# Kernel optimization log

Measured on AMD Instinct MI355X. Metric: run time of the kernel, lower is better.

The kernel has to match this reference:

```python
import jax, jax.numpy as jnp
import numpy as np

MARGIN = 0.0
B, N_CLASSES = 8192, 4


def setup_inputs() -> dict:
    key = jax.random.key(0)
    k1, k2, k3, k4 = jax.random.split(key, 4)
    hazards = jax.random.uniform(k1, (B, N_CLASSES), dtype=jnp.float32)
    S = jax.random.uniform(k2, (B, N_CLASSES), dtype=jnp.float32)
    Y = jax.random.randint(k3, (B,), 0, N_CLASSES, dtype=jnp.int64)
    c = jax.random.randint(k4, (B,), 0, 2, dtype=jnp.int64)
    return {"hazards": hazards, "S": S, "Y": Y, "c": c}


def reference(hazards, S, Y, c):
    # risk score per sample: sum of hazards over time bins
    risk = hazards.sum(axis=1)  # [B]
    # pair (i, j) contributes iff sample i is uncensored and Y[j] > Y[i]
    mask = (c == 0)[:, None] & (Y[None, :] > Y[:, None])  # [B, B] bool
    # diff[i, j] = margin + risk[j] - risk[i]
    diff = jax.nn.relu(MARGIN + risk[None, :] - risk[:, None])  # [B, B]
    count = jnp.sum(mask)
    total = jnp.sum(jnp.where(mask, diff, jnp.zeros_like(diff)))
    # if count == 0, loss stays 0 (matches torch code)
    loss = jnp.where(count > 0, total / count.astype(diff.dtype), jnp.zeros((), diff.dtype))
    return loss
```

## Files before the change

### kernel.cpp

```cpp
#include <hip/hip_runtime.h>


#define B_SIZE 8192
#define TILE 256
#define NBLK ((B_SIZE / TILE) * (B_SIZE / TILE))

__global__ __launch_bounds__(TILE) void rl_pairs(
    const float4* __restrict__ hz,
    const int*    __restrict__ Y,
    const int*    __restrict__ c,
    float*        __restrict__ psum,
    int*          __restrict__ pcnt)
{
    const int tid  = threadIdx.x;
    const int lane = tid & 63;

    const int j = blockIdx.x * TILE + tid;
    const float4 hj = hz[j];
    const float rj = (hj.x + hj.y) + (hj.z + hj.w);
    const int   yj = Y[j];

    const int i0 = blockIdx.y * TILE;
    float ri[4];
    int   yi[4];
    #pragma unroll
    for (int s = 0; s < 4; ++s) {
        const int i = i0 + s * 64 + lane;
        const float4 hi = hz[i];
        ri[s] = (hi.x + hi.y) + (hi.z + hi.w);
        yi[s] = (c[i] != 0) ? 1000 : Y[i];
    }

    float acc = 0.0f;
    int   cnt = 0;
    #pragma unroll
    for (int s = 0; s < 4; ++s) {
        #pragma unroll
        for (int l = 0; l < 64; ++l) {
            const int yib = __builtin_amdgcn_readlane(yi[s], l);
            if (yib < 4) {
                const float rib = __uint_as_float(
                    (unsigned)__builtin_amdgcn_readlane((int)__float_as_uint(ri[s]), l));
                const bool m = (yj > yib);
                const float d = fmaxf(rj - rib, 0.0f);
                acc += m ? d : 0.0f;
                cnt += m ? 1 : 0;
            }
        }
    }

    #pragma unroll
    for (int off = 32; off > 0; off >>= 1) {
        acc += __shfl_down(acc, off, 64);
        cnt += __shfl_down(cnt, off, 64);
    }
    __shared__ float sa[TILE / 64];
    __shared__ int   sc[TILE / 64];
    const int wave = tid >> 6;
    if (lane == 0) { sa[wave] = acc; sc[wave] = cnt; }
    __syncthreads();
    if (tid == 0) {
        float a = 0.0f; int n = 0;
        #pragma unroll
        for (int w = 0; w < TILE / 64; ++w) { a += sa[w]; n += sc[w]; }
        const int gid = blockIdx.y * gridDim.x + blockIdx.x;
        psum[gid] = a;
        pcnt[gid] = n;
    }
}

__global__ __launch_bounds__(256) void rl_final(
    const float* __restrict__ psum,
    const int*   __restrict__ pcnt,
    float*       __restrict__ out)
{
    const int tid  = threadIdx.x;
    const int lane = tid & 63;
    float a = 0.0f; int n = 0;
    #pragma unroll
    for (int k = 0; k < NBLK / 256; ++k) {
        a += psum[k * 256 + tid];
        n += pcnt[k * 256 + tid];
    }
    #pragma unroll
    for (int off = 32; off > 0; off >>= 1) {
        a += __shfl_down(a, off, 64);
        n += __shfl_down(n, off, 64);
    }
    __shared__ float sa[4];
    __shared__ int   sc[4];
    const int wave = tid >> 6;
    if (lane == 0) { sa[wave] = a; sc[wave] = n; }
    __syncthreads();
    if (tid == 0) {
        float A = sa[0] + sa[1] + sa[2] + sa[3];
        int   N = sc[0] + sc[1] + sc[2] + sc[3];
        out[0] = (N > 0) ? (A / (float)N) : 0.0f;
    }
}

extern "C" void kernel_launch(void* const* d_in, const int* in_sizes, int n_in,
                              void* d_out, int out_size, void* d_ws, size_t ws_size,
                              hipStream_t stream) {
    const float4* hz = (const float4*)d_in[0];
    const int* Y = (const int*)d_in[2];
    const int* c = (const int*)d_in[3];
    float* psum = (float*)d_ws;
    int*   pcnt = (int*)d_ws + NBLK;
    float* out  = (float*)d_out;

    rl_pairs<<<dim3(B_SIZE / TILE, B_SIZE / TILE), TILE, 0, stream>>>(hz, Y, c, psum, pcnt);
    rl_final<<<1, 256, 0, stream>>>(psum, pcnt, out);
}
```

Before: 72.86 us.

## Compact uncensored samples by class and compute pair count analytically

Adds a single-block pre-pass that builds per-class histograms of labels, computes the valid-pair count in closed form, and packs uncensored risks into 64-wide class-homogeneous groups padded with sentinels. The pair kernel then loops only over these compacted groups, rotating risks across lanes with DPP moves instead of readlane, and keeps no per-pair count or mask test. This cuts pair work to uncensored samples with smaller labels and removes the counting arithmetic. In exchange it adds an extra serial single-block launch, and a float sentinel trick stands in for the mask.

```diff
diff --git a/kernel.cpp b/kernel.cpp
--- a/kernel.cpp
+++ b/kernel.cpp
@@ -2,100 +2,165 @@
 
 
 #define B_SIZE 8192
-#define TILE 256
-#define NBLK ((B_SIZE / TILE) * (B_SIZE / TILE))
+#define BLOCK  256
+#define JT     (B_SIZE / BLOCK)
+#define GY     32
+#define NPSUM  (JT * GY)
 
-__global__ __launch_bounds__(TILE) void rl_pairs(
+#define CR_OFF    0
+#define GCLS_OFF  36864
+#define SCAL_OFF  40960
+#define PSUM_OFF  49152
+
+__global__ __launch_bounds__(1024) void rl_compact(
     const float4* __restrict__ hz,
     const int*    __restrict__ Y,
     const int*    __restrict__ c,
-    float*        __restrict__ psum,
-    int*          __restrict__ pcnt)
+    float* __restrict__ cr,
+    int*   __restrict__ gcls,
+    int*   __restrict__ scal)
+{
+    const int t    = threadIdx.x;
+    const int lane = t & 63;
+
+    float r[8]; int y[8]; bool keep[8];
+    #pragma unroll
+    for (int k = 0; k < 8; ++k) {
+        const int e = k * 1024 + t;
+        const float4 h = hz[e];
+        r[k] = (h.x + h.y) + (h.z + h.w);
+        y[k] = Y[e];
+        keep[k] = (c[e] == 0);
+    }
+
+    __shared__ int histA[4], histU[4], fill[4];
+    __shared__ int sNG;
+    if (t < 4) { histA[t] = 0; histU[t] = 0; }
+    __syncthreads();
+
+    int la[4] = {0,0,0,0}, lu[4] = {0,0,0,0};
+    #pragma unroll
+    for (int k = 0; k < 8; ++k) {
+        #pragma unroll
+        for (int cls = 0; cls < 4; ++cls) {
+            const unsigned long long mA = __ballot(y[k] == cls);
+            const unsigned long long mU = __ballot(keep[k] && (y[k] == cls));
+            la[cls] += (int)__popcll(mA);
+            lu[cls] += (int)__popcll(mU);
+        }
+    }
+    if (lane == 0) {
+        #pragma unroll
+        for (int cls = 0; cls < 4; ++cls) {
+            atomicAdd(&histA[cls], la[cls]);
+            atomicAdd(&histU[cls], lu[cls]);
+        }
+    }
+    __syncthreads();
+
+    if (t == 0) {
+        int suff[5]; suff[4] = 0;
+        for (int a = 3; a >= 0; --a) suff[a] = suff[a + 1] + histA[a];
+        long long cnt = 0;
+        int off = 0, ng = 0;
+        for (int a = 0; a < 3; ++a) {
+            fill[a] = off;
+            const int pad = (histU[a] + 63) & ~63;
+            for (int g = 0; g < pad / 64; ++g) gcls[ng + g] = a;
+            ng += pad / 64;
+            off += pad;
+            cnt += (long long)histU[a] * suff[a + 1];
+        }
+        cnt += (long long)histU[3] * suff[4];
+        fill[3] = off;
+        sNG = ng;
+        scal[0] = ng;
+        scal[1] = (int)cnt;
+    }
+    __syncthreads();
+
+    const int M = sNG * 64;
+    for (int idx = t; idx < M; idx += 1024) cr[idx] = 1e30f;
+    __syncthreads();
+
+    #pragma unroll
+    for (int k = 0; k < 8; ++k) {
+        #pragma unroll
+        for (int cls = 0; cls < 3; ++cls) {
+            const bool mine = keep[k] && (y[k] == cls);
+            const unsigned long long m = __ballot(mine);
+            if (m == 0ull) continue;
+            const int rank = (int)__popcll(m & ((1ull << lane) - 1ull));
+            int base;
+            if (lane == 0) base = atomicAdd(&fill[cls], (int)__popcll(m));
+            base = __shfl(base, 0, 64);
+            if (mine) cr[base + rank] = r[k];
+        }
+    }
+}
+
+__global__ __launch_bounds__(BLOCK) void rl_pairs(
+    const float4* __restrict__ hz,
+    const int*    __restrict__ Y,
+    const float*  __restrict__ cr,
+    const int*    __restrict__ gcls,
+    const int*    __restrict__ scal,
+    float*        __restrict__ psum)
 {
     const int tid  = threadIdx.x;
     const int lane = tid & 63;
 
-    const int j = blockIdx.x * TILE + tid;
-    const float4 hj = hz[j];
-    const float rj = (hj.x + hj.y) + (hj.z + hj.w);
+    const int j = blockIdx.x * BLOCK + tid;
+    const float4 h = hz[j];
+    const float rj = (h.x + h.y) + (h.z + h.w);
     const int   yj = Y[j];
+    const float rj0 = (yj > 0) ? rj : -1e30f;
+    const float rj1 = (yj > 1) ? rj : -1e30f;
+    const float rj2 = (yj > 2) ? rj : -1e30f;
 
-    const int i0 = blockIdx.y * TILE;
-    float ri[4];
-    int   yi[4];
-    #pragma unroll
-    for (int s = 0; s < 4; ++s) {
-        const int i = i0 + s * 64 + lane;
-        const float4 hi = hz[i];
-        ri[s] = (hi.x + hi.y) + (hi.z + hi.w);
-        yi[s] = (c[i] != 0) ? 1000 : Y[i];
-    }
+    const int NG = scal[0];
+    float acc = 0.0f;
 
-    float acc = 0.0f;
-    int   cnt = 0;
-    #pragma unroll
-    for (int s = 0; s < 4; ++s) {
+    for (int g = blockIdx.y; g < NG; g += GY) {
+        const int cls = gcls[g];
+        const float rjc = (cls == 0) ? rj0 : (cls == 1) ? rj1 : rj2;
+        float ri = cr[g * 64 + lane];
         #pragma unroll
-        for (int l = 0; l < 64; ++l) {
-            const int yib = __builtin_amdgcn_readlane(yi[s], l);
-            if (yib < 4) {
-                const float rib = __uint_as_float(
-                    (unsigned)__builtin_amdgcn_readlane((int)__float_as_uint(ri[s]), l));
-                const bool m = (yj > yib);
-                const float d = fmaxf(rj - rib, 0.0f);
-                acc += m ? d : 0.0f;
-                cnt += m ? 1 : 0;
-            }
+        for (int it = 0; it < 64; ++it) {
+            const float d = rjc - ri;
+            acc += fmaxf(d, 0.0f);
+            ri = __uint_as_float((unsigned)__builtin_amdgcn_mov_dpp(
+                     (int)__float_as_uint(ri), 0x13C , 0xF, 0xF, true));
         }
     }
 
     #pragma unroll
-    for (int off = 32; off > 0; off >>= 1) {
-        acc += __shfl_down(acc, off, 64);
-        cnt += __shfl_down(cnt, off, 64);
-    }
-    __shared__ float sa[TILE / 64];
-    __shared__ int   sc[TILE / 64];
-    const int wave = tid >> 6;
-    if (lane == 0) { sa[wave] = acc; sc[wave] = cnt; }
+    for (int off = 32; off > 0; off >>= 1) acc += __shfl_down(acc, off, 64);
+    __shared__ float sa[BLOCK / 64];
+    if (lane == 0) sa[tid >> 6] = acc;
     __syncthreads();
-    if (tid == 0) {
-        float a = 0.0f; int n = 0;
-        #pragma unroll
-        for (int w = 0; w < TILE / 64; ++w) { a += sa[w]; n += sc[w]; }
-        const int gid = blockIdx.y * gridDim.x + blockIdx.x;
-        psum[gid] = a;
-        pcnt[gid] = n;
-    }
+    if (tid == 0)
+        psum[blockIdx.y * JT + blockIdx.x] = (sa[0] + sa[1]) + (sa[2] + sa[3]);
 }
 
 __global__ __launch_bounds__(256) void rl_final(
     const float* __restrict__ psum,
-    const int*   __restrict__ pcnt,
+    const int*   __restrict__ scal,
     float*       __restrict__ out)
 {
     const int tid  = threadIdx.x;
     const int lane = tid & 63;
-    float a = 0.0f; int n = 0;
+    float a = 0.0f;
     #pragma unroll
-    for (int k = 0; k < NBLK / 256; ++k) {
-        a += psum[k * 256 + tid];
-        n += pcnt[k * 256 + tid];
-    }
+    for (int k = 0; k < NPSUM / 256; ++k) a += psum[k * 256 + tid];
     #pragma unroll
-    for (int off = 32; off > 0; off >>= 1) {
-        a += __shfl_down(a, off, 64);
-        n += __shfl_down(n, off, 64);
-    }
+    for (int off = 32; off > 0; off >>= 1) a += __shfl_down(a, off, 64);
     __shared__ float sa[4];
-    __shared__ int   sc[4];
-    const int wave = tid >> 6;
-    if (lane == 0) { sa[wave] = a; sc[wave] = n; }
+    if (lane == 0) sa[tid >> 6] = a;
     __syncthreads();
     if (tid == 0) {
-        float A = sa[0] + sa[1] + sa[2] + sa[3];
-        int   N = sc[0] + sc[1] + sc[2] + sc[3];
-        out[0] = (N > 0) ? (A / (float)N) : 0.0f;
+        const int n = scal[1];
+        out[0] = (n > 0) ? ((sa[0] + sa[1]) + (sa[2] + sa[3])) / (float)n : 0.0f;
     }
 }
 
@@ -105,10 +170,15 @@
     const float4* hz = (const float4*)d_in[0];
     const int* Y = (const int*)d_in[2];
     const int* c = (const int*)d_in[3];
-    float* psum = (float*)d_ws;
-    int*   pcnt = (int*)d_ws + NBLK;
+
+    char* ws = (char*)d_ws;
+    float* cr   = (float*)(ws + CR_OFF);
+    int*   gcls = (int*)  (ws + GCLS_OFF);
+    int*   scal = (int*)  (ws + SCAL_OFF);
+    float* psum = (float*)(ws + PSUM_OFF);
     float* out  = (float*)d_out;
 
-    rl_pairs<<<dim3(B_SIZE / TILE, B_SIZE / TILE), TILE, 0, stream>>>(hz, Y, c, psum, pcnt);
-    rl_final<<<1, 256, 0, stream>>>(psum, pcnt, out);
+    rl_compact<<<1, 1024, 0, stream>>>(hz, Y, c, cr, gcls, scal);
+    rl_pairs<<<dim3(JT, GY), BLOCK, 0, stream>>>(hz, Y, cr, gcls, scal, psum);
+    rl_final<<<1, 256, 0, stream>>>(psum, scal, out);
 }
```

Measured after the change: 74.63 us. +2.4%, slower.

## Bucket uncensored rows by class in shared memory and compute pair counts analytically

Applied to the files above, without the earlier changes.

Each block now sorts its uncensored i-samples by class into fixed-size shared-memory pads, using ballot, popcount and shared atomics. The pair count becomes a closed-form product of per-class counts and suffix counts instead of per-pair accumulation. The inner loop walks each class pad with DPP wave rotations instead of per-lane readlane plus a branch. Pads are filled with sentinels so unused slots add zero, which removes the masking work and the count accumulation. The trade-off is extra shared atomics and barriers, and each class bucket is capped at 128 entries, so a skewed input could silently drop pairs from the sum.

```diff
diff --git a/kernel.cpp b/kernel.cpp
--- a/kernel.cpp
+++ b/kernel.cpp
@@ -2,70 +2,91 @@
 
 
 #define B_SIZE 8192
-#define TILE 256
-#define NBLK ((B_SIZE / TILE) * (B_SIZE / TILE))
+#define BLOCK  256
+#define JT     (B_SIZE / BLOCK)
+#define IC     (B_SIZE / BLOCK)
+#define NBLK   (JT * IC)
+#define CAP    128
 
-__global__ __launch_bounds__(TILE) void rl_pairs(
+__global__ __launch_bounds__(BLOCK) void rl_all(
     const float4* __restrict__ hz,
     const int*    __restrict__ Y,
     const int*    __restrict__ c,
     float*        __restrict__ psum,
     int*          __restrict__ pcnt)
 {
+    __shared__ float sPad[3 * CAP];
+    __shared__ int   sCnt[3];
+    __shared__ int   sSuf[3];
+    __shared__ float sA[BLOCK / 64];
+    __shared__ int   sN[BLOCK / 64];
+
     const int tid  = threadIdx.x;
     const int lane = tid & 63;
+    const int wave = tid >> 6;
 
-    const int j = blockIdx.x * TILE + tid;
+    if (tid < 3) { sCnt[tid] = 0; sSuf[tid] = 0; }
+    for (int k = tid; k < 3 * CAP; k += BLOCK) sPad[k] = 1e30f;
+
+    const int j = blockIdx.x * BLOCK + tid;
     const float4 hj = hz[j];
     const float rj = (hj.x + hj.y) + (hj.z + hj.w);
     const int   yj = Y[j];
 
-    const int i0 = blockIdx.y * TILE;
-    float ri[4];
-    int   yi[4];
+    const int i = blockIdx.y * BLOCK + tid;
+    const float4 hi = hz[i];
+    const float ri0 = (hi.x + hi.y) + (hi.z + hi.w);
+    const int   yi = Y[i];
+    const bool  keep = (c[i] == 0);
+
+    __syncthreads();
+
     #pragma unroll
-    for (int s = 0; s < 4; ++s) {
-        const int i = i0 + s * 64 + lane;
-        const float4 hi = hz[i];
-        ri[s] = (hi.x + hi.y) + (hi.z + hi.w);
-        yi[s] = (c[i] != 0) ? 1000 : Y[i];
+    for (int cls = 0; cls < 3; ++cls) {
+        const bool mine = keep && (yi == cls);
+        const unsigned long long m = __ballot(mine);
+        if (m) {
+            const int pop  = (int)__popcll(m);
+            const int rank = (int)__popcll(m & ((1ull << lane) - 1ull));
+            int base;
+            if (lane == 0) base = atomicAdd(&sCnt[cls], pop);
+            base = __shfl(base, 0, 64);
+            const int slot = base + rank;
+            if (mine && slot < CAP) sPad[cls * CAP + slot] = ri0;
+        }
+        const unsigned long long mj = __ballot(yj > cls);
+        if (lane == 0 && mj) atomicAdd(&sSuf[cls], (int)__popcll(mj));
     }
+    __syncthreads();
+
+    const float rj0 = (yj > 0) ? rj : -1e30f;
+    const float rj1 = (yj > 1) ? rj : -1e30f;
+    const float rj2 = (yj > 2) ? rj : -1e30f;
 
     float acc = 0.0f;
-    int   cnt = 0;
     #pragma unroll
-    for (int s = 0; s < 4; ++s) {
-        #pragma unroll
-        for (int l = 0; l < 64; ++l) {
-            const int yib = __builtin_amdgcn_readlane(yi[s], l);
-            if (yib < 4) {
-                const float rib = __uint_as_float(
-                    (unsigned)__builtin_amdgcn_readlane((int)__float_as_uint(ri[s]), l));
-                const bool m = (yj > yib);
-                const float d = fmaxf(rj - rib, 0.0f);
-                acc += m ? d : 0.0f;
-                cnt += m ? 1 : 0;
+    for (int cls = 0; cls < 3; ++cls) {
+        const float rjc = (cls == 0) ? rj0 : (cls == 1) ? rj1 : rj2;
+        const int n = min(sCnt[cls], CAP);
+        for (int g = 0; g * 64 < n; ++g) {
+            float ri = sPad[cls * CAP + g * 64 + lane];
+            #pragma unroll
+            for (int it = 0; it < 64; ++it) {
+                acc += fmaxf(rjc - ri, 0.0f);
+                ri = __uint_as_float((unsigned)__builtin_amdgcn_mov_dpp(
+                         (int)__float_as_uint(ri), 0x13C , 0xF, 0xF, true));
             }
         }
     }
 
     #pragma unroll
-    for (int off = 32; off > 0; off >>= 1) {
-        acc += __shfl_down(acc, off, 64);
-        cnt += __shfl_down(cnt, off, 64);
-    }
-    __shared__ float sa[TILE / 64];
-    __shared__ int   sc[TILE / 64];
-    const int wave = tid >> 6;
-    if (lane == 0) { sa[wave] = acc; sc[wave] = cnt; }
+    for (int off = 32; off > 0; off >>= 1) acc += __shfl_down(acc, off, 64);
+    if (lane == 0) sA[wave] = acc;
     __syncthreads();
     if (tid == 0) {
-        float a = 0.0f; int n = 0;
-        #pragma unroll
-        for (int w = 0; w < TILE / 64; ++w) { a += sa[w]; n += sc[w]; }
-        const int gid = blockIdx.y * gridDim.x + blockIdx.x;
-        psum[gid] = a;
-        pcnt[gid] = n;
+        const int gid = blockIdx.y * JT + blockIdx.x;
+        psum[gid] = (sA[0] + sA[1]) + (sA[2] + sA[3]);
+        pcnt[gid] = sCnt[0] * sSuf[0] + sCnt[1] * sSuf[1] + sCnt[2] * sSuf[2];
     }
 }
 
@@ -89,12 +110,11 @@
     }
     __shared__ float sa[4];
     __shared__ int   sc[4];
-    const int wave = tid >> 6;
-    if (lane == 0) { sa[wave] = a; sc[wave] = n; }
+    if (lane == 0) { sa[tid >> 6] = a; sc[tid >> 6] = n; }
     __syncthreads();
     if (tid == 0) {
-        float A = sa[0] + sa[1] + sa[2] + sa[3];
-        int   N = sc[0] + sc[1] + sc[2] + sc[3];
+        const float A = (sa[0] + sa[1]) + (sa[2] + sa[3]);
+        const int   N = (sc[0] + sc[1]) + (sc[2] + sc[3]);
         out[0] = (N > 0) ? (A / (float)N) : 0.0f;
     }
 }
@@ -105,10 +125,11 @@
     const float4* hz = (const float4*)d_in[0];
     const int* Y = (const int*)d_in[2];
     const int* c = (const int*)d_in[3];
+
     float* psum = (float*)d_ws;
     int*   pcnt = (int*)d_ws + NBLK;
     float* out  = (float*)d_out;
 
-    rl_pairs<<<dim3(B_SIZE / TILE, B_SIZE / TILE), TILE, 0, stream>>>(hz, Y, c, psum, pcnt);
+    rl_all<<<dim3(JT, IC), BLOCK, 0, stream>>>(hz, Y, c, psum, pcnt);
     rl_final<<<1, 256, 0, stream>>>(psum, pcnt, out);
 }
```

New measurement: 67.17 us. 1.08x faster.
